# Optimization experiments

Hardware: AMD Instinct MI355X
Metric: run time of the kernel (lower is better)

The kernel has to match this reference:

```python
import jax, jax.numpy as jnp
import numpy as np
import math

N_HEADS = 16
DIM = 1024
D_HEAD = DIM // N_HEADS
BS, QLEN = 2, 2048


def setup_inputs() -> dict:
    key = jax.random.key(0)
    ks = jax.random.split(key, 10)
    s = 0.02
    return {
        "input": jax.random.normal(ks[0], (BS, QLEN, DIM), dtype=jnp.float32),
        "mask": jnp.ones((BS, QLEN), dtype=jnp.int32),
        "q_w": jax.random.normal(ks[1], (DIM, DIM), dtype=jnp.float32) * s,
        "q_b": jax.random.normal(ks[2], (DIM,), dtype=jnp.float32) * s,
        "k_w": jax.random.normal(ks[3], (DIM, DIM), dtype=jnp.float32) * s,
        "k_b": jax.random.normal(ks[4], (DIM,), dtype=jnp.float32) * s,
        "v_w": jax.random.normal(ks[5], (DIM, DIM), dtype=jnp.float32) * s,
        "v_b": jax.random.normal(ks[6], (DIM,), dtype=jnp.float32) * s,
        "o_w": jax.random.normal(ks[7], (DIM, DIM), dtype=jnp.float32) * s,
        "o_b": jax.random.normal(ks[8], (DIM,), dtype=jnp.float32) * s,
    }


def _shape(x, bs):
    # (bs, len, dim) -> (bs, heads, len, d_head)
    return x.reshape(bs, -1, N_HEADS, D_HEAD).transpose(0, 2, 1, 3)


def reference(input, mask, q_w, q_b, k_w, k_b, v_w, v_b, o_w, o_b):
    bs, qlen, dim = input.shape
    # projections (torch Linear: x @ W^T + b)
    q = _shape(input @ q_w.T + q_b, bs)
    k = _shape(input @ k_w.T + k_b, bs)
    v = _shape(input @ v_w.T + v_b, bs)
    q = q / math.sqrt(D_HEAD)
    # scores: (bs, heads, qlen, klen)
    scores = jnp.einsum("bhqd,bhkd->bhqk", q, k)
    pad = (mask == 0)[:, None, None, :]  # (bs,1,1,klen)
    scores = jnp.where(pad, -jnp.inf, scores)
    weights = jax.nn.softmax(scores.astype(jnp.float32), axis=-1).astype(scores.dtype)
    # dropout p=0.0 (eval) -> identity
    context = jnp.einsum("bhqk,bhkd->bhqd", weights, v)
    context = context.transpose(0, 2, 1, 3).reshape(bs, qlen, dim)
    return context @ o_w.T + o_b
```

## Files before the change

kernel.cpp:

```cpp
#include <hip/hip_runtime.h>


#define BS    2
#define QLEN  2048
#define DIM   1024
#define NH    16
#define DH    64
#define MTOK  (BS * QLEN)

#define QSCALE 0.18033688011112042f

typedef __attribute__((ext_vector_type(8))) short short8;
typedef __attribute__((ext_vector_type(4))) float float4_t;
typedef __attribute__((ext_vector_type(4))) int   int4_t;

__device__ __forceinline__ ushort f2bf(float f) {
    unsigned u = __float_as_uint(f);
    return (ushort)((u + 0x7fffu + ((u >> 16) & 1u)) >> 16);
}
__device__ __forceinline__ short8 pack8(float4 a0, float4 a1) {
    short8 r;
    r[0] = (short)f2bf(a0.x); r[1] = (short)f2bf(a0.y);
    r[2] = (short)f2bf(a0.z); r[3] = (short)f2bf(a0.w);
    r[4] = (short)f2bf(a1.x); r[5] = (short)f2bf(a1.y);
    r[6] = (short)f2bf(a1.z); r[7] = (short)f2bf(a1.w);
    return r;
}

__device__ __forceinline__ void glds16(const void* g, void* l) {
    __builtin_amdgcn_global_load_lds(
        (const __attribute__((address_space(1))) unsigned int*)g,
        (__attribute__((address_space(3))) unsigned int*)l, 16, 0, 0);
}

__global__ __launch_bounds__(256) void conv_all(
    const float* __restrict__ x,  const float* __restrict__ qw,
    const float* __restrict__ kw, const float* __restrict__ vw,
    const float* __restrict__ ow,
    ushort* __restrict__ Xbf, ushort* __restrict__ Wbf)
{
    const int blk = blockIdx.x;
    const float* s; ushort* d; size_t base;
    if (blk < 4096)      { s = x;  d = Xbf;             base = (size_t)blk * 1024; }
    else if (blk < 5120) { s = qw; d = Wbf;             base = (size_t)(blk - 4096) * 1024; }
    else if (blk < 6144) { s = kw; d = Wbf + 1048576;   base = (size_t)(blk - 5120) * 1024; }
    else if (blk < 7168) { s = vw; d = Wbf + 2097152;   base = (size_t)(blk - 6144) * 1024; }
    else                 { s = ow; d = Wbf + 3145728;   base = (size_t)(blk - 7168) * 1024; }
    const size_t i = base + threadIdx.x * 4;
    float4 v = *(const float4*)(s + i);
    ushort4 o;
    o.x = f2bf(v.x); o.y = f2bf(v.y); o.z = f2bf(v.z); o.w = f2bf(v.w);
    *(ushort4*)(d + i) = o;
}

__global__ __launch_bounds__(256) void transpose_v(
    const ushort* __restrict__ Vrow, ushort* __restrict__ Vt)
{
    __shared__ ushort T[64][72];
    const int tid  = threadIdx.x;
    const int tile = blockIdx.x;
    const int bh   = blockIdx.y;
    const int b = bh >> 4, h = bh & 15;

    #pragma unroll
    for (int rep = 0; rep < 2; ++rep) {
        int ch = tid + rep * 256;
        int tok = ch >> 3, seg = ch & 7;
        uint4 v = *(const uint4*)(Vrow + (size_t)(b * QLEN + tile * 64 + tok) * DIM
                                        + h * DH + seg * 8);
        *(uint4*)&T[tok][seg * 8] = v;
    }
    __syncthreads();
    #pragma unroll
    for (int rep = 0; rep < 2; ++rep) {
        int ch = tid + rep * 256;
        int dim = ch >> 3, tseg = ch & 7;
        ushort t0 = T[tseg * 8 + 0][dim], t1 = T[tseg * 8 + 1][dim];
        ushort t2 = T[tseg * 8 + 2][dim], t3 = T[tseg * 8 + 3][dim];
        ushort t4 = T[tseg * 8 + 4][dim], t5 = T[tseg * 8 + 5][dim];
        ushort t6 = T[tseg * 8 + 6][dim], t7 = T[tseg * 8 + 7][dim];
        uint4 o;
        o.x = (unsigned)t0 | ((unsigned)t1 << 16);
        o.y = (unsigned)t2 | ((unsigned)t3 << 16);
        o.z = (unsigned)t4 | ((unsigned)t5 << 16);
        o.w = (unsigned)t6 | ((unsigned)t7 << 16);
        *(uint4*)(Vt + (size_t)bh * DH * QLEN + (size_t)dim * QLEN
                      + tile * 64 + tseg * 8) = o;
    }
}

__global__ __launch_bounds__(256) void gemm_qkv(
    const ushort* __restrict__ A, const ushort* __restrict__ Bw,
    const float* __restrict__ bias0, const float* __restrict__ bias1,
    const float* __restrict__ bias2,
    ushort* __restrict__ outQ, ushort* __restrict__ outK, ushort* __restrict__ outVt)
{
    __shared__ ushort As[128 * 64];
    __shared__ ushort Bs[128 * 64];
    const int tid  = threadIdx.x;
    const int w    = tid >> 6;
    const int lane = tid & 63;
    const int r15  = lane & 15;
    const int quad = lane >> 4;
    const int nblk = 3072 >> 7;
    const int brow = blockIdx.x / nblk;
    const int bcol = blockIdx.x - brow * nblk;
    const int wrow = (w >> 1) * 64;
    const int wcol = (w & 1) * 64;
    const int K = DIM;

    float4_t acc[4][4];
    #pragma unroll
    for (int i = 0; i < 4; ++i)
        #pragma unroll
        for (int j = 0; j < 4; ++j)
            acc[i][j] = (float4_t){0.f, 0.f, 0.f, 0.f};

    int chS[4];
    const ushort* gaS[4];
    const ushort* gbS[4];
    #pragma unroll
    for (int rep = 0; rep < 4; ++rep) {
        const int ch  = w * 256 + rep * 64 + lane;
        const int row = ch >> 3;
        const int g   = (ch & 7) ^ (row & 7);
        chS[rep] = ch;
        gaS[rep] = A  + (size_t)(brow * 128 + row) * K + g * 8;
        gbS[rep] = Bw + (size_t)(bcol * 128 + row) * K + g * 8;
    }
    const int xg = r15 & 7;

    for (int k0 = 0; k0 < K; k0 += 64) {
        __syncthreads();
        #pragma unroll
        for (int rep = 0; rep < 4; ++rep) {
            glds16(gaS[rep] + k0, As + chS[rep] * 8);
            glds16(gbS[rep] + k0, Bs + chS[rep] * 8);
        }
        __syncthreads();

        #pragma unroll
        for (int hh = 0; hh < 2; ++hh) {
            const int ph = ((hh * 4 + quad) ^ xg) * 8;
            short8 af[4], bf[4];
            #pragma unroll
            for (int ms = 0; ms < 4; ++ms)
                af[ms] = *(const short8*)&As[(wrow + ms * 16 + r15) * 64 + ph];
            #pragma unroll
            for (int ns = 0; ns < 4; ++ns)
                bf[ns] = *(const short8*)&Bs[(wcol + ns * 16 + r15) * 64 + ph];
            #pragma unroll
            for (int ms = 0; ms < 4; ++ms)
                #pragma unroll
                for (int ns = 0; ns < 4; ++ns)
                    acc[ms][ns] = __builtin_amdgcn_mfma_f32_16x16x32_bf16(
                        af[ms], bf[ns], acc[ms][ns], 0, 0, 0);
        }
    }

    #pragma unroll
    for (int ms = 0; ms < 4; ++ms) {
        const int rowg = brow * 128 + wrow + ms * 16 + quad * 4;
        #pragma unroll
        for (int ns = 0; ns < 4; ++ns) {
            const int colg = bcol * 128 + wcol + ns * 16 + r15;
            if (colg < 1024) {
                const float bb = bias0[colg];
                #pragma unroll
                for (int r = 0; r < 4; ++r)
                    outQ[(size_t)(rowg + r) * 1024 + colg] =
                        f2bf((acc[ms][ns][r] + bb) * QSCALE);
            } else if (colg < 2048) {
                const float bb = bias1[colg - 1024];
                #pragma unroll
                for (int r = 0; r < 4; ++r)
                    outK[(size_t)(rowg + r) * 1024 + (colg - 1024)] =
                        f2bf(acc[ms][ns][r] + bb);
            } else {
                const int vcol = colg - 2048;
                const int hh = vcol >> 6, dd = vcol & 63;
                const float bb = bias2[vcol];
                const int bidx = rowg >> 11;
                const int tloc = rowg & 2047;
                ushort4 o4;
                o4.x = f2bf(acc[ms][ns][0] + bb);
                o4.y = f2bf(acc[ms][ns][1] + bb);
                o4.z = f2bf(acc[ms][ns][2] + bb);
                o4.w = f2bf(acc[ms][ns][3] + bb);
                *(ushort4*)&outVt[((size_t)(bidx * 16 + hh) * 64 + dd) * QLEN + tloc] = o4;
            }
        }
    }
}

__global__ __launch_bounds__(256) void gemm_o(
    const ushort* __restrict__ A, const ushort* __restrict__ Bw,
    const float* __restrict__ bias, float* __restrict__ Out)
{
    __shared__ ushort As[128 * 64];
    __shared__ ushort Bs[64 * 64];
    const int tid  = threadIdx.x;
    const int w    = tid >> 6;
    const int lane = tid & 63;
    const int r15  = lane & 15;
    const int quad = lane >> 4;
    const int brow = blockIdx.x >> 4;
    const int bcol = blockIdx.x & 15;
    const int wrow = w * 32;
    const int K = DIM;

    float4_t acc[2][4];
    #pragma unroll
    for (int i = 0; i < 2; ++i)
        #pragma unroll
        for (int j = 0; j < 4; ++j)
            acc[i][j] = (float4_t){0.f, 0.f, 0.f, 0.f};

    int chA[4];  const ushort* gaS[4];
    #pragma unroll
    for (int rep = 0; rep < 4; ++rep) {
        const int ch  = w * 256 + rep * 64 + lane;
        const int row = ch >> 3;
        const int g   = (ch & 7) ^ (row & 7);
        chA[rep] = ch;
        gaS[rep] = A + (size_t)(brow * 128 + row) * K + g * 8;
    }
    int chB[2];  const ushort* gbS[2];
    #pragma unroll
    for (int rep = 0; rep < 2; ++rep) {
        const int ch  = w * 128 + rep * 64 + lane;
        const int row = ch >> 3;
        const int g   = (ch & 7) ^ (row & 7);
        chB[rep] = ch;
        gbS[rep] = Bw + (size_t)(bcol * 64 + row) * K + g * 8;
    }
    const int xg = r15 & 7;

    for (int k0 = 0; k0 < K; k0 += 64) {
        __syncthreads();
        #pragma unroll
        for (int rep = 0; rep < 4; ++rep)
            glds16(gaS[rep] + k0, As + chA[rep] * 8);
        #pragma unroll
        for (int rep = 0; rep < 2; ++rep)
            glds16(gbS[rep] + k0, Bs + chB[rep] * 8);
        __syncthreads();

        #pragma unroll
        for (int hh = 0; hh < 2; ++hh) {
            const int ph = ((hh * 4 + quad) ^ xg) * 8;
            short8 af[2], bf[4];
            #pragma unroll
            for (int ms = 0; ms < 2; ++ms)
                af[ms] = *(const short8*)&As[(wrow + ms * 16 + r15) * 64 + ph];
            #pragma unroll
            for (int ns = 0; ns < 4; ++ns)
                bf[ns] = *(const short8*)&Bs[(ns * 16 + r15) * 64 + ph];
            #pragma unroll
            for (int ms = 0; ms < 2; ++ms)
                #pragma unroll
                for (int ns = 0; ns < 4; ++ns)
                    acc[ms][ns] = __builtin_amdgcn_mfma_f32_16x16x32_bf16(
                        af[ms], bf[ns], acc[ms][ns], 0, 0, 0);
        }
    }

    #pragma unroll
    for (int ms = 0; ms < 2; ++ms) {
        const int rowg = brow * 128 + wrow + ms * 16 + quad * 4;
        #pragma unroll
        for (int ns = 0; ns < 4; ++ns) {
            const int colg = bcol * 64 + ns * 16 + r15;
            const float bb = bias[colg];
            #pragma unroll
            for (int r = 0; r < 4; ++r)
                Out[(size_t)(rowg + r) * 1024 + colg] = acc[ms][ns][r] + bb;
        }
    }
}

__global__ __launch_bounds__(256) void gemm_f32in_bf16out(
    const float* __restrict__ X, const float* __restrict__ W,
    const float* __restrict__ B, ushort* __restrict__ Out,
    int M, int N, int K, float scale)
{
    const int lane = threadIdx.x & 63;
    const int wid  = (blockIdx.x * blockDim.x + threadIdx.x) >> 6;
    const int tilesN = N >> 4;
    const int tm = wid / tilesN;
    const int tn = wid - tm * tilesN;
    const int r15  = lane & 15;
    const int quad = lane >> 4;

    const float* xp = X + (size_t)(tm * 16 + r15) * K + quad * 8;
    const float* wp = W + (size_t)(tn * 16 + r15) * K + quad * 8;

    float4_t acc = {0.f, 0.f, 0.f, 0.f};
    for (int k0 = 0; k0 < K; k0 += 32) {
        float4 a0 = *(const float4*)(xp + k0);
        float4 a1 = *(const float4*)(xp + k0 + 4);
        float4 b0 = *(const float4*)(wp + k0);
        float4 b1 = *(const float4*)(wp + k0 + 4);
        acc = __builtin_amdgcn_mfma_f32_16x16x32_bf16(pack8(a0, a1), pack8(b0, b1), acc, 0, 0, 0);
    }
    const int col  = tn * 16 + r15;
    const float bias = B[col];
    const int row0 = tm * 16 + quad * 4;
    #pragma unroll
    for (int r = 0; r < 4; ++r)
        Out[(size_t)(row0 + r) * N + col] = f2bf((acc[r] + bias) * scale);
}

__global__ __launch_bounds__(256) void gemm_bf16in_f32out(
    const ushort* __restrict__ X, const float* __restrict__ W,
    const float* __restrict__ B, float* __restrict__ Out,
    int M, int N, int K)
{
    const int lane = threadIdx.x & 63;
    const int wid  = (blockIdx.x * blockDim.x + threadIdx.x) >> 6;
    const int tilesN = N >> 4;
    const int tm = wid / tilesN;
    const int tn = wid - tm * tilesN;
    const int r15  = lane & 15;
    const int quad = lane >> 4;

    const ushort* xp = X + (size_t)(tm * 16 + r15) * K + quad * 8;
    const float*  wp = W + (size_t)(tn * 16 + r15) * K + quad * 8;

    float4_t acc = {0.f, 0.f, 0.f, 0.f};
    for (int k0 = 0; k0 < K; k0 += 32) {
        short8 a = *(const short8*)(xp + k0);
        float4 b0 = *(const float4*)(wp + k0);
        float4 b1 = *(const float4*)(wp + k0 + 4);
        acc = __builtin_amdgcn_mfma_f32_16x16x32_bf16(a, pack8(b0, b1), acc, 0, 0, 0);
    }
    const int col  = tn * 16 + r15;
    const float bias = B[col];
    const int row0 = tm * 16 + quad * 4;
    #pragma unroll
    for (int r = 0; r < 4; ++r)
        Out[(size_t)(row0 + r) * N + col] = acc[r] + bias;
}

__global__ __launch_bounds__(256) void flash_attn(
    const ushort* __restrict__ Qb, const ushort* __restrict__ Kb,
    const ushort* __restrict__ Vt, const int* __restrict__ mask,
    ushort* __restrict__ Cb)
{
    __shared__ __align__(16) ushort Ks[2][64][64];
    __shared__ __align__(16) ushort Vs[2][64][64];
    __shared__ __align__(16) float  Mb[QLEN];

    const int tid  = threadIdx.x;
    const int w    = tid >> 6;
    const int lane = tid & 63;
    const int r15  = lane & 15;
    const int quad = lane >> 4;
    const int bh = blockIdx.y;
    const int b = bh >> 4, h = bh & 15;

    {
        const int4* m4 = (const int4*)(mask + b * QLEN);
        #pragma unroll
        for (int rep = 0; rep < 2; ++rep) {
            const int idx = tid + rep * 256;
            int4 mv = m4[idx];
            float4 o;
            o.x = mv.x ? 0.f : -INFINITY;
            o.y = mv.y ? 0.f : -INFINITY;
            o.z = mv.z ? 0.f : -INFINITY;
            o.w = mv.w ? 0.f : -INFINITY;
            *(float4*)&Mb[idx * 4] = o;
        }
    }

    const int qbase = blockIdx.x * 128 + w * 32;
    const ushort* qp = Qb + (size_t)(b * QLEN + qbase + r15) * DIM + h * DH + quad * 8;
    short8 qf[2][2];
    qf[0][0] = *(const short8*)(qp);
    qf[0][1] = *(const short8*)(qp + 32);
    qf[1][0] = *(const short8*)(qp + 16 * DIM);
    qf[1][1] = *(const short8*)(qp + 16 * DIM + 32);

    const ushort* kg = Kb + (size_t)b * QLEN * DIM + h * DH;
    const ushort* vg = Vt + (size_t)bh * DH * QLEN;

    const int a0 = tid >> 3, seg = tid & 7;
    const int krow0 = (((a0 & 7) >> 2) << 4) + (((a0 >> 3) & 3) << 2) + (a0 & 3);
    const int sK = (seg ^ (krow0 & 7)) << 3;
    const int sV = (seg ^ (a0 & 7)) << 3;
    const int xq = (quad ^ (r15 & 7)) << 3;

    float4_t o[2][4];
    float4_t ol[2];
    #pragma unroll
    for (int rg = 0; rg < 2; ++rg) {
        ol[rg] = (float4_t){0.f, 0.f, 0.f, 0.f};
        #pragma unroll
        for (int ds = 0; ds < 4; ++ds)
            o[rg][ds] = (float4_t){0.f, 0.f, 0.f, 0.f};
    }
    short8 ones8;
    #pragma unroll
    for (int i = 0; i < 8; ++i) ones8[i] = (short)0x3F80;

    uint4 kr0 = *(const uint4*)(kg + (size_t)(a0     ) * DIM + seg * 8);
    uint4 kr1 = *(const uint4*)(kg + (size_t)(a0 + 32) * DIM + seg * 8);
    uint4 vr0 = *(const uint4*)(vg + (size_t)(a0     ) * QLEN + seg * 8);
    uint4 vr1 = *(const uint4*)(vg + (size_t)(a0 + 32) * QLEN + seg * 8);
    *(uint4*)&Ks[0][krow0     ][sK] = kr0;
    *(uint4*)&Ks[0][krow0 + 32][sK] = kr1;
    *(uint4*)&Vs[0][a0        ][sV] = vr0;
    *(uint4*)&Vs[0][a0 + 32   ][sV] = vr1;
    __syncthreads();

    int p = 0;
    for (int kt = 0; kt < QLEN; kt += 64) {
        const bool more = (kt + 64 < QLEN);
        if (more) {
            kr0 = *(const uint4*)(kg + (size_t)(kt + 64 + a0     ) * DIM + seg * 8);
            kr1 = *(const uint4*)(kg + (size_t)(kt + 64 + a0 + 32) * DIM + seg * 8);
            vr0 = *(const uint4*)(vg + (size_t)(a0     ) * QLEN + kt + 64 + seg * 8);
            vr1 = *(const uint4*)(vg + (size_t)(a0 + 32) * QLEN + kt + 64 + seg * 8);
        }

        int pk[4][2][2];
        #pragma unroll
        for (int ks = 0; ks < 4; ++ks) {
            const ushort* krow = &Ks[p][ks * 16 + r15][0];
            short8 kf0 = *(const short8*)(krow + xq);
            short8 kf1 = *(const short8*)(krow + (xq ^ 32));
            const float4 mb = *(const float4*)&Mb[kt + ((ks >> 1) << 5)
                                                   + (quad << 3) + ((ks & 1) << 2)];
            #pragma unroll
            for (int rg = 0; rg < 2; ++rg) {
                float4_t s = {0.f, 0.f, 0.f, 0.f};
                s = __builtin_amdgcn_mfma_f32_16x16x32_bf16(kf0, qf[rg][0], s, 0, 0, 0);
                s = __builtin_amdgcn_mfma_f32_16x16x32_bf16(kf1, qf[rg][1], s, 0, 0, 0);
                unsigned u0 = __float_as_uint(__builtin_amdgcn_exp2f(s[0] + mb.x));
                unsigned u1 = __float_as_uint(__builtin_amdgcn_exp2f(s[1] + mb.y));
                unsigned u2 = __float_as_uint(__builtin_amdgcn_exp2f(s[2] + mb.z));
                unsigned u3 = __float_as_uint(__builtin_amdgcn_exp2f(s[3] + mb.w));
                pk[ks][rg][0] = __builtin_amdgcn_perm(u1, u0, 0x07060302);
                pk[ks][rg][1] = __builtin_amdgcn_perm(u3, u2, 0x07060302);
            }
        }

        #pragma unroll
        for (int ck = 0; ck < 2; ++ck) {
            short8 vf[4];
            #pragma unroll
            for (int ds = 0; ds < 4; ++ds)
                vf[ds] = *(const short8*)(&Vs[p][ds * 16 + r15][0] + (xq ^ (ck << 5)));
            #pragma unroll
            for (int rg = 0; rg < 2; ++rg) {
                int4_t pfi = { pk[2 * ck][rg][0], pk[2 * ck][rg][1],
                               pk[2 * ck + 1][rg][0], pk[2 * ck + 1][rg][1] };
                short8 pf = __builtin_bit_cast(short8, pfi);
                #pragma unroll
                for (int ds = 0; ds < 4; ++ds)
                    o[rg][ds] = __builtin_amdgcn_mfma_f32_16x16x32_bf16(
                        pf, vf[ds], o[rg][ds], 0, 0, 0);
                ol[rg] = __builtin_amdgcn_mfma_f32_16x16x32_bf16(
                    pf, ones8, ol[rg], 0, 0, 0);
            }
        }

        if (more) {
            *(uint4*)&Ks[p ^ 1][krow0     ][sK] = kr0;
            *(uint4*)&Ks[p ^ 1][krow0 + 32][sK] = kr1;
            *(uint4*)&Vs[p ^ 1][a0        ][sV] = vr0;
            *(uint4*)&Vs[p ^ 1][a0 + 32   ][sV] = vr1;
        }
        __syncthreads();
        p ^= 1;
    }

    #pragma unroll
    for (int rg = 0; rg < 2; ++rg) {
        #pragma unroll
        for (int r = 0; r < 4; ++r) {
            const float ir = 1.f / fmaxf(ol[rg][r], 1e-30f);
            const size_t rb = (size_t)(b * QLEN + qbase + rg * 16 + quad * 4 + r) * DIM
                              + h * DH;
            Cb[rb +  0 + r15] = f2bf(o[rg][0][r] * ir);
            Cb[rb + 16 + r15] = f2bf(o[rg][1][r] * ir);
            Cb[rb + 32 + r15] = f2bf(o[rg][2][r] * ir);
            Cb[rb + 48 + r15] = f2bf(o[rg][3][r] * ir);
        }
    }
}

extern "C" void kernel_launch(void* const* d_in, const int* in_sizes, int n_in,
                              void* d_out, int out_size, void* d_ws, size_t ws_size,
                              hipStream_t stream)
{
    const float* x    = (const float*)d_in[0];
    const int*   mask = (const int*)d_in[1];
    const float* q_w  = (const float*)d_in[2];
    const float* q_b  = (const float*)d_in[3];
    const float* k_w  = (const float*)d_in[4];
    const float* k_b  = (const float*)d_in[5];
    const float* v_w  = (const float*)d_in[6];
    const float* v_b  = (const float*)d_in[7];
    const float* o_w  = (const float*)d_in[8];
    const float* o_b  = (const float*)d_in[9];
    float* out = (float*)d_out;

    const size_t SEG = (size_t)MTOK * DIM;
    ushort* Qbf = (ushort*)d_out;
    ushort* Xbf = Qbf + SEG;
    ushort* Kb  = (ushort*)d_ws;
    ushort* Cb  = Kb + SEG;
    ushort* Vt  = Cb + SEG;
    ushort* Wbf = Vt + SEG;

    const bool big = ws_size >= (size_t)32 * 1024 * 1024;

    if (big) {
        conv_all<<<8192, 256, 0, stream>>>(x, q_w, k_w, v_w, o_w, Xbf, Wbf);
        gemm_qkv<<<(MTOK / 128) * (3072 / 128), 256, 0, stream>>>(
            Xbf, Wbf, q_b, k_b, v_b, Qbf, Kb, Vt);
        flash_attn<<<dim3(QLEN / 128, BS * NH), 256, 0, stream>>>(Qbf, Kb, Vt, mask, Cb);
        gemm_o<<<(MTOK / 128) * (DIM / 64), 256, 0, stream>>>(
            Cb, Wbf + 3 * (size_t)(DIM * DIM), o_b, out);
    } else {
        const int tiles   = (MTOK / 16) * (DIM / 16);
        const int gblocks = tiles / 4;
        gemm_f32in_bf16out<<<gblocks, 256, 0, stream>>>(x, q_w, q_b, Qbf, MTOK, DIM, DIM, QSCALE);
        gemm_f32in_bf16out<<<gblocks, 256, 0, stream>>>(x, k_w, k_b, Kb,  MTOK, DIM, DIM, 1.0f);
        gemm_f32in_bf16out<<<gblocks, 256, 0, stream>>>(x, v_w, v_b, Cb,  MTOK, DIM, DIM, 1.0f);
        transpose_v<<<dim3(QLEN / 64, BS * NH), 256, 0, stream>>>(Cb, Vt);
        flash_attn<<<dim3(QLEN / 128, BS * NH), 256, 0, stream>>>(Qbf, Kb, Vt, mask, Cb);
        gemm_bf16in_f32out<<<tiles / 4, 256, 0, stream>>>(Cb, o_w, o_b, out, MTOK, DIM, DIM);
    }
}
```

Measured before the change: 199.7 us.

## Software-pipeline flash attention: overlap QK^T/exp of next tile with PV of current

Restructures the flash attention key loop into a software pipeline where the score MFMA and exp for tile i+1 run alongside the PV MFMAs for tile i, using two register sets of packed probabilities. V now rotates through four LDS buffers while K keeps two, and the loop is manually unrolled by four with explicit prologue and epilogue. Launch bounds add a minimum of two blocks per SIMD/CU hint. This aims to hide exp latency and LDS waits behind matrix work, but it adds register pressure from the doubled pk arrays and more LDS use, which could lower occupancy or cause spills.

Result: faster. 194.8 us (-2.4%).

```diff
diff --git a/kernel.cpp b/kernel.cpp
--- a/kernel.cpp
+++ b/kernel.cpp
@@ -342,13 +342,13 @@
         Out[(size_t)(row0 + r) * N + col] = acc[r] + bias;
 }
 
-__global__ __launch_bounds__(256) void flash_attn(
+__global__ __launch_bounds__(256, 2) void flash_attn(
     const ushort* __restrict__ Qb, const ushort* __restrict__ Kb,
     const ushort* __restrict__ Vt, const int* __restrict__ mask,
     ushort* __restrict__ Cb)
 {
     __shared__ __align__(16) ushort Ks[2][64][64];
-    __shared__ __align__(16) ushort Vs[2][64][64];
+    __shared__ __align__(16) ushort Vs[4][64][64];
     __shared__ __align__(16) float  Mb[QLEN];
 
     const int tid  = threadIdx.x;
@@ -404,77 +404,99 @@
     #pragma unroll
     for (int i = 0; i < 8; ++i) ones8[i] = (short)0x3F80;
 
-    uint4 kr0 = *(const uint4*)(kg + (size_t)(a0     ) * DIM + seg * 8);
-    uint4 kr1 = *(const uint4*)(kg + (size_t)(a0 + 32) * DIM + seg * 8);
-    uint4 vr0 = *(const uint4*)(vg + (size_t)(a0     ) * QLEN + seg * 8);
-    uint4 vr1 = *(const uint4*)(vg + (size_t)(a0 + 32) * QLEN + seg * 8);
-    *(uint4*)&Ks[0][krow0     ][sK] = kr0;
-    *(uint4*)&Ks[0][krow0 + 32][sK] = kr1;
-    *(uint4*)&Vs[0][a0        ][sV] = vr0;
-    *(uint4*)&Vs[0][a0 + 32   ][sV] = vr1;
+    uint4 kr0, kr1, vr0, vr1;
+    int pkA[4][2][2], pkB[4][2][2];
+
+#define LOAD_TILE(KT) do {                                                    \
+    kr0 = *(const uint4*)(kg + (size_t)((KT) + a0     ) * DIM  + seg * 8);    \
+    kr1 = *(const uint4*)(kg + (size_t)((KT) + a0 + 32) * DIM  + seg * 8);    \
+    vr0 = *(const uint4*)(vg + (size_t)(a0     ) * QLEN + (KT) + seg * 8);    \
+    vr1 = *(const uint4*)(vg + (size_t)(a0 + 32) * QLEN + (KT) + seg * 8);    \
+} while (0)
+
+#define STORE_TILE(KBUF, VBUF) do {                                           \
+    *(uint4*)&Ks[KBUF][krow0     ][sK] = kr0;                                 \
+    *(uint4*)&Ks[KBUF][krow0 + 32][sK] = kr1;                                 \
+    *(uint4*)&Vs[VBUF][a0        ][sV] = vr0;                                 \
+    *(uint4*)&Vs[VBUF][a0 + 32   ][sV] = vr1;                                 \
+} while (0)
+
+#define S_PHASE(KBUF, KT, PK) do {                                            \
+    _Pragma("unroll")                                                         \
+    for (int ks = 0; ks < 4; ++ks) {                                          \
+        const ushort* krow = &Ks[KBUF][ks * 16 + r15][0];                     \
+        short8 kf0 = *(const short8*)(krow + xq);                             \
+        short8 kf1 = *(const short8*)(krow + (xq ^ 32));                      \
+        const float4 mb = *(const float4*)&Mb[(KT) + ((ks >> 1) << 5)         \
+                                              + (quad << 3) + ((ks & 1) << 2)]; \
+        _Pragma("unroll")                                                     \
+        for (int rg = 0; rg < 2; ++rg) {                                      \
+            float4_t s = {0.f, 0.f, 0.f, 0.f};                                \
+            s = __builtin_amdgcn_mfma_f32_16x16x32_bf16(kf0, qf[rg][0], s, 0, 0, 0); \
+            s = __builtin_amdgcn_mfma_f32_16x16x32_bf16(kf1, qf[rg][1], s, 0, 0, 0); \
+            unsigned u0 = __float_as_uint(__builtin_amdgcn_exp2f(s[0] + mb.x)); \
+            unsigned u1 = __float_as_uint(__builtin_amdgcn_exp2f(s[1] + mb.y)); \
+            unsigned u2 = __float_as_uint(__builtin_amdgcn_exp2f(s[2] + mb.z)); \
+            unsigned u3 = __float_as_uint(__builtin_amdgcn_exp2f(s[3] + mb.w)); \
+            PK[ks][rg][0] = __builtin_amdgcn_perm(u1, u0, 0x07060302);        \
+            PK[ks][rg][1] = __builtin_amdgcn_perm(u3, u2, 0x07060302);        \
+        }                                                                     \
+    }                                                                         \
+} while (0)
+
+#define PV_PHASE(VBUF, PK) do {                                               \
+    _Pragma("unroll")                                                         \
+    for (int ck = 0; ck < 2; ++ck) {                                          \
+        short8 vf[4];                                                         \
+        _Pragma("unroll")                                                     \
+        for (int ds = 0; ds < 4; ++ds)                                        \
+            vf[ds] = *(const short8*)(&Vs[VBUF][ds * 16 + r15][0] + (xq ^ (ck << 5))); \
+        _Pragma("unroll")                                                     \
+        for (int rg = 0; rg < 2; ++rg) {                                      \
+            int4_t pfi = { PK[2 * ck][rg][0], PK[2 * ck][rg][1],              \
+                           PK[2 * ck + 1][rg][0], PK[2 * ck + 1][rg][1] };    \
+            short8 pf = __builtin_bit_cast(short8, pfi);                      \
+            _Pragma("unroll")                                                 \
+            for (int ds = 0; ds < 4; ++ds)                                    \
+                o[rg][ds] = __builtin_amdgcn_mfma_f32_16x16x32_bf16(          \
+                    pf, vf[ds], o[rg][ds], 0, 0, 0);                          \
+            ol[rg] = __builtin_amdgcn_mfma_f32_16x16x32_bf16(                 \
+                pf, ones8, ol[rg], 0, 0, 0);                                  \
+        }                                                                     \
+    }                                                                         \
+} while (0)
+
+    LOAD_TILE(0);
+    STORE_TILE(0, 0);
+    LOAD_TILE(64);
     __syncthreads();
-
-    int p = 0;
-    for (int kt = 0; kt < QLEN; kt += 64) {
-        const bool more = (kt + 64 < QLEN);
-        if (more) {
-            kr0 = *(const uint4*)(kg + (size_t)(kt + 64 + a0     ) * DIM + seg * 8);
-            kr1 = *(const uint4*)(kg + (size_t)(kt + 64 + a0 + 32) * DIM + seg * 8);
-            vr0 = *(const uint4*)(vg + (size_t)(a0     ) * QLEN + kt + 64 + seg * 8);
-            vr1 = *(const uint4*)(vg + (size_t)(a0 + 32) * QLEN + kt + 64 + seg * 8);
-        }
-
-        int pk[4][2][2];
-        #pragma unroll
-        for (int ks = 0; ks < 4; ++ks) {
-            const ushort* krow = &Ks[p][ks * 16 + r15][0];
-            short8 kf0 = *(const short8*)(krow + xq);
-            short8 kf1 = *(const short8*)(krow + (xq ^ 32));
-            const float4 mb = *(const float4*)&Mb[kt + ((ks >> 1) << 5)
-                                                   + (quad << 3) + ((ks & 1) << 2)];
-            #pragma unroll
-            for (int rg = 0; rg < 2; ++rg) {
-                float4_t s = {0.f, 0.f, 0.f, 0.f};
-                s = __builtin_amdgcn_mfma_f32_16x16x32_bf16(kf0, qf[rg][0], s, 0, 0, 0);
-                s = __builtin_amdgcn_mfma_f32_16x16x32_bf16(kf1, qf[rg][1], s, 0, 0, 0);
-                unsigned u0 = __float_as_uint(__builtin_amdgcn_exp2f(s[0] + mb.x));
-                unsigned u1 = __float_as_uint(__builtin_amdgcn_exp2f(s[1] + mb.y));
-                unsigned u2 = __float_as_uint(__builtin_amdgcn_exp2f(s[2] + mb.z));
-                unsigned u3 = __float_as_uint(__builtin_amdgcn_exp2f(s[3] + mb.w));
-                pk[ks][rg][0] = __builtin_amdgcn_perm(u1, u0, 0x07060302);
-                pk[ks][rg][1] = __builtin_amdgcn_perm(u3, u2, 0x07060302);
-            }
-        }
-
-        #pragma unroll
-        for (int ck = 0; ck < 2; ++ck) {
-            short8 vf[4];
-            #pragma unroll
-            for (int ds = 0; ds < 4; ++ds)
-                vf[ds] = *(const short8*)(&Vs[p][ds * 16 + r15][0] + (xq ^ (ck << 5)));
-            #pragma unroll
-            for (int rg = 0; rg < 2; ++rg) {
-                int4_t pfi = { pk[2 * ck][rg][0], pk[2 * ck][rg][1],
-                               pk[2 * ck + 1][rg][0], pk[2 * ck + 1][rg][1] };
-                short8 pf = __builtin_bit_cast(short8, pfi);
-                #pragma unroll
-                for (int ds = 0; ds < 4; ++ds)
-                    o[rg][ds] = __builtin_amdgcn_mfma_f32_16x16x32_bf16(
-                        pf, vf[ds], o[rg][ds], 0, 0, 0);
-                ol[rg] = __builtin_amdgcn_mfma_f32_16x16x32_bf16(
-                    pf, ones8, ol[rg], 0, 0, 0);
-            }
-        }
-
-        if (more) {
-            *(uint4*)&Ks[p ^ 1][krow0     ][sK] = kr0;
-            *(uint4*)&Ks[p ^ 1][krow0 + 32][sK] = kr1;
-            *(uint4*)&Vs[p ^ 1][a0        ][sV] = vr0;
-            *(uint4*)&Vs[p ^ 1][a0 + 32   ][sV] = vr1;
-        }
-        __syncthreads();
-        p ^= 1;
-    }
+    S_PHASE(0, 0, pkA);
+    STORE_TILE(1, 1);
+    __syncthreads();
+    LOAD_TILE(128);
+
+    for (int kb = 0; kb < 1792; kb += 256) {
+        S_PHASE(1, kb + 64, pkB);  PV_PHASE(0, pkA);
+        STORE_TILE(0, 2); __syncthreads(); LOAD_TILE(kb + 192);
+        S_PHASE(0, kb + 128, pkA); PV_PHASE(1, pkB);
+        STORE_TILE(1, 3); __syncthreads(); LOAD_TILE(kb + 256);
+        S_PHASE(1, kb + 192, pkB); PV_PHASE(2, pkA);
+        STORE_TILE(0, 0); __syncthreads(); LOAD_TILE(kb + 320);
+        S_PHASE(0, kb + 256, pkA); PV_PHASE(3, pkB);
+        STORE_TILE(1, 1); __syncthreads(); LOAD_TILE(kb + 384);
+    }
+
+    S_PHASE(1, 1856, pkB); PV_PHASE(0, pkA);
+    STORE_TILE(0, 2); __syncthreads(); LOAD_TILE(1984);
+    S_PHASE(0, 1920, pkA); PV_PHASE(1, pkB);
+    STORE_TILE(1, 3); __syncthreads();
+    S_PHASE(1, 1984, pkB); PV_PHASE(2, pkA);
+    PV_PHASE(3, pkB);
+
+#undef LOAD_TILE
+#undef STORE_TILE
+#undef S_PHASE
+#undef PV_PHASE
 
     #pragma unroll
     for (int rg = 0; rg < 2; ++rg) {
```
